# Optimization experiments

Hardware: AMD Instinct MI355X
Metric: run time of the kernel (lower is better)

Reference implementation:

```python
import jax, jax.numpy as jnp
import numpy as np

K = 31            # kernel_size
P = K // 2        # padding
EPS = 1e-05
STRENGTH = 1.0


def _box_filter(x):
    """31x31 mean box filter with zero padding, done as two separable 1D passes.
    Exactly equals F.conv2d(x, ones(K,K)/K^2, padding=P) since the box kernel
    is separable and padding is zero-fill."""
    kh = jnp.ones((1, 1, K, 1), x.dtype) / K  # vertical pass
    kw = jnp.ones((1, 1, 1, K), x.dtype) / K  # horizontal pass
    dn = jax.lax.conv_dimension_numbers(x.shape, kh.shape, ('NCHW', 'OIHW', 'NCHW'))
    x = jax.lax.conv_general_dilated(x, kh, (1, 1), [(P, P), (0, 0)], dimension_numbers=dn)
    x = jax.lax.conv_general_dilated(x, kw, (1, 1), [(0, 0), (P, P)], dimension_numbers=dn)
    return x


def setup_inputs() -> dict:
    key = jax.random.key(0)
    # (B, 1, H, W) image in [0, 1]
    x = jax.random.uniform(key, (32, 1, 1024, 1024), dtype=jnp.float32)
    return {"x": x}


def reference(x):
    local_mean = _box_filter(x)
    local_sq_mean = _box_filter(x * x)
    local_var = local_sq_mean - local_mean * local_mean
    local_std = jnp.sqrt(jnp.maximum(local_var, EPS))  # clamp(min=eps) then sqrt
    normalized = (x - local_mean) / (local_std + EPS)
    enhanced = jax.nn.sigmoid(normalized * 0.5)
    return x * (1.0 - STRENGTH) + enhanced * STRENGTH
```

## Files before the change

kernel.cpp:

```cpp
#include <hip/hip_runtime.h>
#include <math.h>


#define KSZ    31
#define PAD    15
#define IMG_H  1024
#define IMG_W  1024
#define SH     32
#define RPP    4
#define PHASES (SH / RPP)
#define NT     256
#define LROW   66
#define LBUF   (16 * LROW)
#define EPSV   1e-5f

__global__ __launch_bounds__(NT, 4)
void lcn_fused_kernel(const float* __restrict__ x, float* __restrict__ out) {
    const int cpx = gridDim.x >> 3;
    const int bid = (blockIdx.x & 7) * cpx + (blockIdx.x >> 3);

    const int chunk = bid & 31;
    const int b     = bid >> 5;
    const int y0    = chunk * SH;

    const float* img  = x   + (size_t)b * (IMG_H * IMG_W);
    float*       oimg = out + (size_t)b * (IMG_H * IMG_W);

    __shared__ float2 vbuf[RPP][LBUF];

    const int t    = threadIdx.x;
    const int wave = t >> 6;
    const int lane = t & 63;

    for (int i = t; i < RPP * 32; i += NT) {
        const int r = i >> 5, k = i & 31;
        float2* vb = vbuf[r];
        if (k < 16) vb[k * LROW] = make_float2(0.f, 0.f);
        else        vb[(k - 16) * LROW + (LROW - 1)] = make_float2(0.f, 0.f);
    }

    const int c0 = 4 * t;
    float vs0 = 0.f, vs1 = 0.f, vs2 = 0.f, vs3 = 0.f;
    float vq0 = 0.f, vq1 = 0.f, vq2 = 0.f, vq3 = 0.f;
    for (int y = y0 - PAD; y <= y0 + PAD; ++y) {
        const int yc = max(y, 0);
        float4 v = *(const float4*)(img + (size_t)yc * IMG_W + c0);
        const float m = (y >= 0) ? 1.f : 0.f;
        v.x *= m; v.y *= m; v.z *= m; v.w *= m;
        vs0 += v.x; vq0 = fmaf(v.x, v.x, vq0);
        vs1 += v.y; vq1 = fmaf(v.y, v.y, vq1);
        vs2 += v.z; vq2 = fmaf(v.z, v.z, vq2);
        vs3 += v.w; vq3 = fmaf(v.w, v.w, vq3);
    }

    int wp0, wp1, wp2, wp3;
    {
        const int iv = c0 + 16;
        wp0 = ((iv    ) & 15) * LROW + ((iv    ) >> 4);
        wp1 = ((iv + 1) & 15) * LROW + ((iv + 1) >> 4);
        wp2 = ((iv + 2) & 15) * LROW + ((iv + 2) >> 4);
        wp3 = ((iv + 3) & 15) * LROW + ((iv + 3) >> 4);
    }

    const int   cbase = lane << 4;
    const float inv   = 1.0f / 961.0f;

    float4 sb[RPP], ad[RPP];
    float4 xa, xb, xc, xd;
    {
        #pragma unroll
        for (int r = 0; r < RPP; ++r) {
            const int ys = y0 + r - PAD;
            const int ya = y0 + r + PAD + 1;
            const int ysc = max(ys, 0);
            float4 vS = *(const float4*)(img + (size_t)ysc * IMG_W + c0);
            float4 vA = *(const float4*)(img + (size_t)ya  * IMG_W + c0);
            const float mS = (ys >= 0) ? 1.f : 0.f;
            vS.x *= mS; vS.y *= mS; vS.z *= mS; vS.w *= mS;
            sb[r] = vS; ad[r] = vA;
        }
        const float* xr = img + (size_t)(y0 + wave) * IMG_W + cbase;
        xa = ((const float4*)xr)[0]; xb = ((const float4*)xr)[1];
        xc = ((const float4*)xr)[2]; xd = ((const float4*)xr)[3];
    }

    __syncthreads();

    for (int ph = 0; ph < PHASES; ++ph) {
        const int yo = y0 + ph * RPP;

        #pragma unroll
        for (int r = 0; r < RPP; ++r) {
            vbuf[r][wp0] = make_float2(vs0, vq0);
            vbuf[r][wp1] = make_float2(vs1, vq1);
            vbuf[r][wp2] = make_float2(vs2, vq2);
            vbuf[r][wp3] = make_float2(vs3, vq3);
            vs0 += ad[r].x - sb[r].x;
            vq0 = fmaf(ad[r].x, ad[r].x, vq0); vq0 = fmaf(-sb[r].x, sb[r].x, vq0);
            vs1 += ad[r].y - sb[r].y;
            vq1 = fmaf(ad[r].y, ad[r].y, vq1); vq1 = fmaf(-sb[r].y, sb[r].y, vq1);
            vs2 += ad[r].z - sb[r].z;
            vq2 = fmaf(ad[r].z, ad[r].z, vq2); vq2 = fmaf(-sb[r].z, sb[r].z, vq2);
            vs3 += ad[r].w - sb[r].w;
            vq3 = fmaf(ad[r].w, ad[r].w, vq3); vq3 = fmaf(-sb[r].w, sb[r].w, vq3);
        }
        __syncthreads();

        if (ph < PHASES - 1) {
            const int yn = yo + RPP;
            #pragma unroll
            for (int r = 0; r < RPP; ++r) {
                const int ys = yn + r - PAD;
                const int ya = yn + r + PAD + 1;
                const int ysc = max(ys, 0);
                const int yac = min(ya, IMG_H - 1);
                float4 vS = *(const float4*)(img + (size_t)ysc * IMG_W + c0);
                float4 vA = *(const float4*)(img + (size_t)yac * IMG_W + c0);
                const float mS = (ys >= 0)    ? 1.f : 0.f;
                const float mA = (ya < IMG_H) ? 1.f : 0.f;
                vS.x *= mS; vS.y *= mS; vS.z *= mS; vS.w *= mS;
                vA.x *= mA; vA.y *= mA; vA.z *= mA; vA.w *= mA;
                sb[r] = vS; ad[r] = vA;
            }
        }
        float4 nxa, nxb, nxc, nxd;
        if (ph < PHASES - 1) {
            const float* xr = img + (size_t)(yo + RPP + wave) * IMG_W + cbase;
            nxa = ((const float4*)xr)[0]; nxb = ((const float4*)xr)[1];
            nxc = ((const float4*)xr)[2]; nxd = ((const float4*)xr)[3];
        }

        {
            const float2* vr = &vbuf[wave][lane];
            float hs = 0.f, hq = 0.f;
            #pragma unroll
            for (int s = 1; s <= 31; ++s) {
                float2 v = vr[(s & 15) * LROW + (s >> 4)];
                hs += v.x; hq += v.y;
            }
            float xs[16] = { xa.x, xa.y, xa.z, xa.w,  xb.x, xb.y, xb.z, xb.w,
                             xc.x, xc.y, xc.z, xc.w,  xd.x, xd.y, xd.z, xd.w };
            float res[16];
            #pragma unroll
            for (int j = 0; j < 16; ++j) {
                if (j > 0) {
                    float2 va  = vr[((j - 1) & 15) * LROW + 2];
                    float2 vsu = vr[(j & 15) * LROW];
                    hs += va.x - vsu.x;
                    hq += va.y - vsu.y;
                }
                const float mean = hs * inv;
                const float var  = fmaf(-mean, mean, hq * inv);
                const float stdv = sqrtf(fmaxf(var, EPSV));
                const float norm = (xs[j] - mean) *
                                   __builtin_amdgcn_rcpf(stdv + EPSV);
                res[j] = __builtin_amdgcn_rcpf(1.0f + __expf(-0.5f * norm));
            }
            float* orow = oimg + (size_t)(yo + wave) * IMG_W + cbase;
            ((float4*)orow)[0] = make_float4(res[0],  res[1],  res[2],  res[3]);
            ((float4*)orow)[1] = make_float4(res[4],  res[5],  res[6],  res[7]);
            ((float4*)orow)[2] = make_float4(res[8],  res[9],  res[10], res[11]);
            ((float4*)orow)[3] = make_float4(res[12], res[13], res[14], res[15]);
        }

        xa = nxa; xb = nxb; xc = nxc; xd = nxd;
        __syncthreads();
    }
}

extern "C" void kernel_launch(void* const* d_in, const int* in_sizes, int n_in,
                              void* d_out, int out_size, void* d_ws, size_t ws_size,
                              hipStream_t stream) {
    (void)n_in; (void)out_size; (void)d_ws; (void)ws_size;
    const float* x = (const float*)d_in[0];
    float* out = (float*)d_out;
    const int B = in_sizes[0] / (IMG_H * IMG_W);
    dim3 grid(B * (IMG_H / SH));
    lcn_fused_kernel<<<grid, NT, 0, stream>>>(x, out);
}
```

Measured before the change: 101.1 us.

## Use 64-row strips with 512 threads and 2 columns per thread, drop prefetch

Each block now covers 64 output rows with 512 threads. Each thread keeps vertical running sums for 2 columns instead of 4, and 8 rows are processed per phase so the 8 waves each compute one row. Taller strips cut how often the 30-row vertical halo is re-read per output row. Register prefetch of the next phase's rows is removed and loads now happen inside each phase, which lowers register pressure but exposes global load latency before each phase's compute.

```diff
diff --git a/kernel.cpp b/kernel.cpp
--- a/kernel.cpp
+++ b/kernel.cpp
@@ -6,10 +6,10 @@
 #define PAD    15
 #define IMG_H  1024
 #define IMG_W  1024
-#define SH     32
-#define RPP    4
+#define SH     64
+#define RPP    8
 #define PHASES (SH / RPP)
-#define NT     256
+#define NT     512
 #define LROW   66
 #define LBUF   (16 * LROW)
 #define EPSV   1e-5f
@@ -19,8 +19,8 @@
     const int cpx = gridDim.x >> 3;
     const int bid = (blockIdx.x & 7) * cpx + (blockIdx.x >> 3);
 
-    const int chunk = bid & 31;
-    const int b     = bid >> 5;
+    const int chunk = bid & 15;
+    const int b     = bid >> 4;
     const int y0    = chunk * SH;
 
     const float* img  = x   + (size_t)b * (IMG_H * IMG_W);
@@ -39,98 +39,55 @@
         else        vb[(k - 16) * LROW + (LROW - 1)] = make_float2(0.f, 0.f);
     }
 
-    const int c0 = 4 * t;
-    float vs0 = 0.f, vs1 = 0.f, vs2 = 0.f, vs3 = 0.f;
-    float vq0 = 0.f, vq1 = 0.f, vq2 = 0.f, vq3 = 0.f;
+    const int c0 = 2 * t;
+    float vs0 = 0.f, vs1 = 0.f, vq0 = 0.f, vq1 = 0.f;
     for (int y = y0 - PAD; y <= y0 + PAD; ++y) {
         const int yc = max(y, 0);
-        float4 v = *(const float4*)(img + (size_t)yc * IMG_W + c0);
+        float2 v = *(const float2*)(img + (size_t)yc * IMG_W + c0);
         const float m = (y >= 0) ? 1.f : 0.f;
-        v.x *= m; v.y *= m; v.z *= m; v.w *= m;
+        v.x *= m; v.y *= m;
         vs0 += v.x; vq0 = fmaf(v.x, v.x, vq0);
         vs1 += v.y; vq1 = fmaf(v.y, v.y, vq1);
-        vs2 += v.z; vq2 = fmaf(v.z, v.z, vq2);
-        vs3 += v.w; vq3 = fmaf(v.w, v.w, vq3);
     }
 
-    int wp0, wp1, wp2, wp3;
-    {
-        const int iv = c0 + 16;
-        wp0 = ((iv    ) & 15) * LROW + ((iv    ) >> 4);
-        wp1 = ((iv + 1) & 15) * LROW + ((iv + 1) >> 4);
-        wp2 = ((iv + 2) & 15) * LROW + ((iv + 2) >> 4);
-        wp3 = ((iv + 3) & 15) * LROW + ((iv + 3) >> 4);
-    }
+    const int iv0 = c0 + 16;
+    const int wp0 = ((iv0    ) & 15) * LROW + ((iv0    ) >> 4);
+    const int wp1 = ((iv0 + 1) & 15) * LROW + ((iv0 + 1) >> 4);
 
     const int   cbase = lane << 4;
     const float inv   = 1.0f / 961.0f;
 
-    float4 sb[RPP], ad[RPP];
-    float4 xa, xb, xc, xd;
-    {
+    for (int ph = 0; ph < PHASES; ++ph) {
+        const int yo = y0 + ph * RPP;
+
+        float2 sb[RPP], ad[RPP];
         #pragma unroll
         for (int r = 0; r < RPP; ++r) {
-            const int ys = y0 + r - PAD;
-            const int ya = y0 + r + PAD + 1;
+            const int ys  = yo + r - PAD;
+            const int ya  = yo + r + PAD + 1;
             const int ysc = max(ys, 0);
-            float4 vS = *(const float4*)(img + (size_t)ysc * IMG_W + c0);
-            float4 vA = *(const float4*)(img + (size_t)ya  * IMG_W + c0);
-            const float mS = (ys >= 0) ? 1.f : 0.f;
-            vS.x *= mS; vS.y *= mS; vS.z *= mS; vS.w *= mS;
-            sb[r] = vS; ad[r] = vA;
+            const int yac = min(ya, IMG_H - 1);
+            float2 vS = *(const float2*)(img + (size_t)ysc * IMG_W + c0);
+            float2 vA = *(const float2*)(img + (size_t)yac * IMG_W + c0);
+            const float mS = (ys >= 0)    ? 1.f : 0.f;
+            const float mA = (ya < IMG_H) ? 1.f : 0.f;
+            sb[r] = make_float2(vS.x * mS, vS.y * mS);
+            ad[r] = make_float2(vA.x * mA, vA.y * mA);
         }
-        const float* xr = img + (size_t)(y0 + wave) * IMG_W + cbase;
-        xa = ((const float4*)xr)[0]; xb = ((const float4*)xr)[1];
-        xc = ((const float4*)xr)[2]; xd = ((const float4*)xr)[3];
-    }
-
-    __syncthreads();
-
-    for (int ph = 0; ph < PHASES; ++ph) {
-        const int yo = y0 + ph * RPP;
 
         #pragma unroll
         for (int r = 0; r < RPP; ++r) {
             vbuf[r][wp0] = make_float2(vs0, vq0);
             vbuf[r][wp1] = make_float2(vs1, vq1);
-            vbuf[r][wp2] = make_float2(vs2, vq2);
-            vbuf[r][wp3] = make_float2(vs3, vq3);
             vs0 += ad[r].x - sb[r].x;
             vq0 = fmaf(ad[r].x, ad[r].x, vq0); vq0 = fmaf(-sb[r].x, sb[r].x, vq0);
             vs1 += ad[r].y - sb[r].y;
             vq1 = fmaf(ad[r].y, ad[r].y, vq1); vq1 = fmaf(-sb[r].y, sb[r].y, vq1);
-            vs2 += ad[r].z - sb[r].z;
-            vq2 = fmaf(ad[r].z, ad[r].z, vq2); vq2 = fmaf(-sb[r].z, sb[r].z, vq2);
-            vs3 += ad[r].w - sb[r].w;
-            vq3 = fmaf(ad[r].w, ad[r].w, vq3); vq3 = fmaf(-sb[r].w, sb[r].w, vq3);
         }
         __syncthreads();
 
-        if (ph < PHASES - 1) {
-            const int yn = yo + RPP;
-            #pragma unroll
-            for (int r = 0; r < RPP; ++r) {
-                const int ys = yn + r - PAD;
-                const int ya = yn + r + PAD + 1;
-                const int ysc = max(ys, 0);
-                const int yac = min(ya, IMG_H - 1);
-                float4 vS = *(const float4*)(img + (size_t)ysc * IMG_W + c0);
-                float4 vA = *(const float4*)(img + (size_t)yac * IMG_W + c0);
-                const float mS = (ys >= 0)    ? 1.f : 0.f;
-                const float mA = (ya < IMG_H) ? 1.f : 0.f;
-                vS.x *= mS; vS.y *= mS; vS.z *= mS; vS.w *= mS;
-                vA.x *= mA; vA.y *= mA; vA.z *= mA; vA.w *= mA;
-                sb[r] = vS; ad[r] = vA;
-            }
-        }
-        float4 nxa, nxb, nxc, nxd;
-        if (ph < PHASES - 1) {
-            const float* xr = img + (size_t)(yo + RPP + wave) * IMG_W + cbase;
-            nxa = ((const float4*)xr)[0]; nxb = ((const float4*)xr)[1];
-            nxc = ((const float4*)xr)[2]; nxd = ((const float4*)xr)[3];
-        }
-
         {
+            const int row = yo + wave;
             const float2* vr = &vbuf[wave][lane];
             float hs = 0.f, hq = 0.f;
             #pragma unroll
@@ -138,6 +95,11 @@
                 float2 v = vr[(s & 15) * LROW + (s >> 4)];
                 hs += v.x; hq += v.y;
             }
+            const float* xr = img + (size_t)row * IMG_W + cbase;
+            float4 xa = ((const float4*)xr)[0];
+            float4 xb = ((const float4*)xr)[1];
+            float4 xc = ((const float4*)xr)[2];
+            float4 xd = ((const float4*)xr)[3];
             float xs[16] = { xa.x, xa.y, xa.z, xa.w,  xb.x, xb.y, xb.z, xb.w,
                              xc.x, xc.y, xc.z, xc.w,  xd.x, xd.y, xd.z, xd.w };
             float res[16];
@@ -156,14 +118,12 @@
                                    __builtin_amdgcn_rcpf(stdv + EPSV);
                 res[j] = __builtin_amdgcn_rcpf(1.0f + __expf(-0.5f * norm));
             }
-            float* orow = oimg + (size_t)(yo + wave) * IMG_W + cbase;
+            float* orow = oimg + (size_t)row * IMG_W + cbase;
             ((float4*)orow)[0] = make_float4(res[0],  res[1],  res[2],  res[3]);
             ((float4*)orow)[1] = make_float4(res[4],  res[5],  res[6],  res[7]);
             ((float4*)orow)[2] = make_float4(res[8],  res[9],  res[10], res[11]);
             ((float4*)orow)[3] = make_float4(res[12], res[13], res[14], res[15]);
         }
-
-        xa = nxa; xb = nxb; xc = nxc; xd = nxd;
         __syncthreads();
     }
 }
```

New measurement: 89.67 us. 11.3% less time.
